# Optimization experiments

Hardware: AMD Instinct MI355X
Metric: run time of the kernel (lower is better)

The kernel has to match this reference:

```python
import jax, jax.numpy as jnp
import numpy as np

LOCAL_RADIUS = 127          # block_len = 128
TOKENS_PER_BLOCK = 16       # global_seq_len = L // 16
NEG = -1e9


def _concat_3_blocks(x):
    # x: [B, nb, bl, H, d] -> [B, nb, 3*bl, H, d] (prev, cur, next block; zero-padded ends)
    p = jnp.pad(x, [(0, 0), (1, 1), (0, 0), (0, 0), (0, 0)])
    return jnp.concatenate([p[:, :-2], p[:, 1:-1], p[:, 2:]], axis=2)


def _softmax_with_extra_logit(x, axis=-1):
    m = jnp.maximum(jax.lax.stop_gradient(x.max(axis, keepdims=True)), 0)
    unnorm = jnp.exp(x - m)
    denom = unnorm.sum(axis, keepdims=True) + jnp.exp(-m)
    return unnorm / denom


def setup_inputs() -> dict:
    key = jax.random.key(0)
    ks = jax.random.split(key, 5)
    B, L, D, H, dh = 2, 4096, 1024, 16, 64
    return {
        "x": jax.random.normal(ks[0], (B, L, D), jnp.float32),
        "Wq": jax.random.normal(ks[1], (D, H, dh), jnp.float32) * 0.02,
        "Wk": jax.random.normal(ks[2], (D, H, dh), jnp.float32) * 0.02,
        "Wv": jax.random.normal(ks[3], (D, H, dh), jnp.float32) * 0.02,
        "Wo": jax.random.normal(ks[4], (H, dh, D), jnp.float32) * 0.02,
    }


def reference(x, Wq, Wk, Wv, Wo):
    B, L, D = x.shape
    H, dh = Wq.shape[1], Wq.shape[2]
    bl = LOCAL_RADIUS + 1                      # block_len = 128
    nb = L // bl                               # num_blocks
    G = L // TOKENS_PER_BLOCK                  # global (side) seq len

    q = jnp.einsum("bld,dhk->blhk", x, Wq) / jnp.sqrt(jnp.asarray(dh, x.dtype))
    k = jnp.einsum("bld,dhk->blhk", x, Wk)
    v = jnp.einsum("bld,dhk->blhk", x, Wv)

    # transient-global aggregates: sum token embeddings within each block of TOKENS_PER_BLOCK
    block_ids = jnp.arange(L) // TOKENS_PER_BLOCK          # [L]
    one_hot = jax.nn.one_hot(block_ids, G, dtype=x.dtype)  # [L, G]
    g = jnp.einsum("bld,lg->bgd", x, one_hot)              # [B, G, D]
    side_k = jnp.einsum("bgd,dhk->bghk", g, Wk)
    side_v = jnp.einsum("bgd,dhk->bghk", g, Wv)

    # split into blocks and build 3-block sliding window keys/values
    qb = q.reshape(B, nb, bl, H, dh)
    kb = _concat_3_blocks(k.reshape(B, nb, bl, H, dh))     # [B, nb, 3bl, H, dh]
    vb = _concat_3_blocks(v.reshape(B, nb, bl, H, dh))

    k_cat = jnp.concatenate(
        [kb, jnp.broadcast_to(side_k[:, None], (B, nb, G, H, dh))], axis=2)
    v_cat = jnp.concatenate(
        [vb, jnp.broadcast_to(side_v[:, None], (B, nb, G, H, dh))], axis=2)

    # logits: [B, nb, H, bl, 3bl+G]
    logits = jnp.einsum("bnqhd,bnkhd->bnhqk", qb, k_cat)

    # local mask: enforce |rel| <= local_radius and in-bounds key positions
    q_idx = jnp.arange(bl)[:, None]                        # [bl, 1]
    k_idx = jnp.arange(3 * bl)[None, :]                    # [1, 3bl]
    rel = k_idx - bl - q_idx                               # relative position
    b_idx = jnp.arange(nb)[:, None, None]                  # [nb, 1, 1]
    k_pos = (b_idx - 1) * bl + k_idx                       # absolute key position
    valid = (jnp.abs(rel) <= LOCAL_RADIUS) & (k_pos >= 0) & (k_pos < L)
    local_bias = jnp.where(valid, 0.0, NEG).astype(logits.dtype)  # [nb, bl, 3bl]
    side_bias = jnp.zeros((nb, bl, G), logits.dtype)
    bias = jnp.concatenate([local_bias, side_bias], axis=-1)      # [nb, bl, 3bl+G]
    logits = logits + bias[None, :, None]

    probs = _softmax_with_extra_logit(logits, axis=-1)
    y = jnp.einsum("bnhqk,bnkhd->bnqhd", probs, v_cat)
    y = y.reshape(B, L, H, dh)
    return jnp.einsum("blhk,hkd->bld", y, Wo)
```

## Files before the change

kernel.cpp:

```cpp
#include <hip/hip_runtime.h>
#include <stdint.h>

#define SC_LOG2E 0.18033688011112042f

typedef __attribute__((ext_vector_type(8))) short short8;
typedef __attribute__((ext_vector_type(4))) short short4v;
typedef __attribute__((ext_vector_type(4))) float f32x4;

__device__ __forceinline__ unsigned short f2bf(float f) {
  unsigned int u = __float_as_uint(f);
  u += 0x7fffu + ((u >> 16) & 1u);
  return (unsigned short)(u >> 16);
}

__device__ __forceinline__ float bf2f(unsigned short u) {
  return __uint_as_float(((unsigned int)u) << 16);
}

__device__ __forceinline__ void gload_lds16(const void* g, void* l) {
  __builtin_amdgcn_global_load_lds((const __attribute__((address_space(1))) void*)g,
                                   (__attribute__((address_space(3))) void*)l,
                                   16, 0, 0);
}

__device__ __forceinline__ f32x4 mfma16(short8 a, short8 b, f32x4 c) {
  return __builtin_amdgcn_mfma_f32_16x16x32_bf16(a, b, c, 0, 0, 0);
}

__device__ __forceinline__ short4v tr_read(const unsigned short* p) {
  short4v r;
  asm volatile("ds_read_b64_tr_b16 %0, %1"
               : "=v"(r)
               : "v"((const __attribute__((address_space(3))) unsigned short*)p));
  return r;
}

__device__ __forceinline__ short8 cat44(short4v lo, short4v hi) {
  return __builtin_shufflevector(lo, hi, 0, 1, 2, 3, 4, 5, 6, 7);
}

__global__ __launch_bounds__(256) void prep_k(
    const float* __restrict__ x, unsigned short* __restrict__ xb,
    const float* __restrict__ wq, const float* __restrict__ wk,
    const float* __restrict__ wv, const float* __restrict__ wo,
    unsigned short* __restrict__ wqkv_t, unsigned short* __restrict__ wo_t) {
  __shared__ float tile[64 * 65];
  int bid = blockIdx.x;
  if (bid < 512) {
    int gr = bid;
    int c4 = threadIdx.x;
    const float4* p = (const float4*)(x + (size_t)gr * 16384) + c4;
#pragma unroll
    for (int t = 0; t < 16; ++t) {
      float4 v = p[(size_t)t * 256];
      ushort4 o;
      o.x = f2bf(v.x); o.y = f2bf(v.y); o.z = f2bf(v.z); o.w = f2bf(v.w);
      ((ushort4*)xb)[(size_t)(gr * 16 + t) * 256 + c4] = o;
    }
  } else {
    int idx = bid - 512;
    int z = idx >> 8, rem = idx & 255;
    const float* src = (z == 0) ? wq : (z == 1) ? wk : (z == 2) ? wv : wo;
    unsigned short* dst = (z == 3) ? wo_t : (wqkv_t + (size_t)z * 1048576);
    float scale = (z == 0) ? SC_LOG2E : 1.0f;
    int tc = (rem & 15) * 64, tr = (rem >> 4) * 64;
    int cx = threadIdx.x & 63, ry = threadIdx.x >> 6;
#pragma unroll
    for (int i = 0; i < 16; ++i) {
      int r = ry + i * 4;
      tile[r * 65 + cx] = src[(size_t)(tr + r) * 1024 + tc + cx];
    }
    __syncthreads();
#pragma unroll
    for (int i = 0; i < 16; ++i) {
      int r = ry + i * 4;
      dst[(size_t)(tc + r) * 1024 + tr + cx] = f2bf(tile[cx * 65 + r] * scale);
    }
  }
}

__global__ __launch_bounds__(256) void side_sum_k(
    const unsigned short* __restrict__ qkvb, unsigned short* __restrict__ sidekv) {
  int gr = blockIdx.x;
  int c8 = threadIdx.x;
  const unsigned short* src = qkvb + (size_t)(gr * 16) * 3072 + 1024 + c8 * 8;
  float s[8];
#pragma unroll
  for (int j = 0; j < 8; ++j) s[j] = 0.f;
#pragma unroll
  for (int t = 0; t < 16; ++t) {
    short8 v = *(const short8*)(src + (size_t)t * 3072);
#pragma unroll
    for (int j = 0; j < 8; ++j) s[j] += bf2f((unsigned short)v[j]);
  }
  short8 o;
#pragma unroll
  for (int j = 0; j < 8; ++j) o[j] = (short)f2bf(s[j]);
  *(short8*)(sidekv + (size_t)gr * 2048 + c8 * 8) = o;
}

template <bool F32OUT>
__global__ __launch_bounds__(256) void gemm_bt_k(
    const unsigned short* __restrict__ A, const unsigned short* __restrict__ Bt,
    void* __restrict__ Cv, int M, int N, int K, int nbn) {
  __shared__ unsigned short Alds[128 * 64];
  __shared__ unsigned short Blds[128 * 64];
  int bid = blockIdx.x;
  int bm = bid / nbn, bn = bid % nbn;
  int lane = threadIdx.x & 63, wid = threadIdx.x >> 6;
  int wr = wid >> 1, wc = wid & 1;
  int l15 = lane & 15, lg = lane >> 4;

  f32x4 zero4 = {0.f, 0.f, 0.f, 0.f};
  f32x4 acc[4][4];
#pragma unroll
  for (int i = 0; i < 4; ++i)
#pragma unroll
    for (int j = 0; j < 4; ++j) acc[i][j] = zero4;

  int srow[4], scol[4];
#pragma unroll
  for (int i = 0; i < 4; ++i) {
    int seg = wid * 4 + i;
    int r = seg * 8 + (lane >> 3);
    srow[i] = r;
    scol[i] = ((lane & 7) ^ (r & 7)) * 8;
  }
  size_t arow0 = (size_t)bm * 128, brow0 = (size_t)bn * 128;

  int ksteps = K >> 6;
  for (int ks = 0; ks < ksteps; ++ks) {
    int k0 = ks << 6;
#pragma unroll
    for (int i = 0; i < 4; ++i) {
      gload_lds16(A + (arow0 + srow[i]) * K + k0 + scol[i],
                  (char*)Alds + (wid * 4 + i) * 1024);
      gload_lds16(Bt + (brow0 + srow[i]) * K + k0 + scol[i],
                  (char*)Blds + (wid * 4 + i) * 1024);
    }
    __syncthreads();
#pragma unroll
    for (int kk = 0; kk < 2; ++kk) {
      short8 af[4], bfr[4];
#pragma unroll
      for (int mi = 0; mi < 4; ++mi) {
        int r = wr * 64 + mi * 16 + l15;
        af[mi] = *(const short8*)((const char*)Alds + r * 128 +
                                  ((kk * 64 + lg * 16) ^ ((r & 7) << 4)));
      }
#pragma unroll
      for (int ni = 0; ni < 4; ++ni) {
        int r = wc * 64 + ni * 16 + l15;
        bfr[ni] = *(const short8*)((const char*)Blds + r * 128 +
                                   ((kk * 64 + lg * 16) ^ ((r & 7) << 4)));
      }
#pragma unroll
      for (int mi = 0; mi < 4; ++mi)
#pragma unroll
        for (int ni = 0; ni < 4; ++ni)
          acc[mi][ni] = mfma16(af[mi], bfr[ni], acc[mi][ni]);
    }
    __syncthreads();
  }
  int rq = lg << 2;
#pragma unroll
  for (int mi = 0; mi < 4; ++mi) {
    size_t row = arow0 + wr * 64 + mi * 16 + rq;
#pragma unroll
    for (int ni = 0; ni < 4; ++ni) {
      size_t col = brow0 + wc * 64 + ni * 16 + l15;
#pragma unroll
      for (int r = 0; r < 4; ++r) {
        if (F32OUT)
          ((float*)Cv)[(row + r) * N + col] = acc[mi][ni][r];
        else
          ((unsigned short*)Cv)[(row + r) * N + col] = f2bf(acc[mi][ni][r]);
      }
    }
  }
}

__global__ __launch_bounds__(256) void attn_k(
    const unsigned short* __restrict__ qkv,
    const unsigned short* __restrict__ side,
    unsigned short* __restrict__ y) {
  const int L = 4096, G = 256;
  __shared__ unsigned short K0[4096], V0[4096];
  __shared__ unsigned short K1[4096], V1[4096];
  __shared__ unsigned short Pt[4][1024];

  int bid = blockIdx.x;
  int n = bid & 31, h = (bid >> 5) & 15, b = bid >> 9;
  int lane = threadIdx.x & 63, wid = threadIdx.x >> 6;
  int l15 = lane & 15, lg = lane >> 4, rq = lg << 2;

  short8 qf[2][2];
  {
    size_t rowb = (size_t)b * L + n * 128 + wid * 32;
#pragma unroll
    for (int qt = 0; qt < 2; ++qt)
#pragma unroll
      for (int kk = 0; kk < 2; ++kk)
        qf[qt][kk] = *(const short8*)(qkv + (rowb + qt * 16 + l15) * 3072 +
                                      h * 64 + kk * 32 + lg * 8);
  }

  f32x4 zero4 = {0.f, 0.f, 0.f, 0.f};
  f32x4 accO[2][4], accSum[2];
#pragma unroll
  for (int qt = 0; qt < 2; ++qt) {
    accSum[qt] = zero4;
#pragma unroll
    for (int dt = 0; dt < 4; ++dt) accO[qt][dt] = zero4;
  }

  short8 onesf;
  {
    short o = (l15 == 0) ? (short)0x3F80 : (short)0;
    onesf = (short8){o, o, o, o, o, o, o, o};
  }

  int clo = (n == 0) ? 2 : 0, chi = (n == 31) ? 4 : 6;
  int nloc = chi - clo, goff = 6 - nloc;
  int m = nloc + 4;
  unsigned short* pt = Pt[wid];

  auto stage = [&](int c, unsigned short* Kl, unsigned short* Vl) {
    bool isg = c >= 6;
#pragma unroll
    for (int i = 0; i < 2; ++i) {
      int seg = wid * 2 + i;
      int r = seg * 8 + (lane >> 3);
      int sl = ((lane & 7) ^ (r & 7)) * 8;
      int S = seg * 8 + (lane >> 3);
      int di = S >> 4, ks = (S >> 3) & 1, lgg = (S >> 1) & 3, half = S & 1;
      int k = ks * 32 + lgg * 8 + half * 4 + ((lane & 7) >> 1);
      int d = di * 16 + (lane & 1) * 8;
      const unsigned short *ksrc, *vsrc;
      if (!isg) {
        int rowbase = b * L + (n - 1) * 128 + c * 64;
        ksrc = qkv + (size_t)(rowbase + r) * 3072 + 1024 + h * 64 + sl;
        vsrc = qkv + (size_t)(rowbase + k) * 3072 + 2048 + h * 64 + d;
      } else {
        int rowbase = b * G + (c - 6) * 64;
        ksrc = side + (size_t)(rowbase + r) * 2048 + h * 64 + sl;
        vsrc = side + (size_t)(rowbase + k) * 2048 + 1024 + h * 64 + d;
      }
      gload_lds16(ksrc, (char*)Kl + seg * 1024);
      gload_lds16(vsrc, (char*)Vl + seg * 1024);
    }
  };

  auto compute = [&](int c, const unsigned short* Kl, const unsigned short* Vl) {
    bool isg = c >= 6;
    int d0 = c * 64 - 128 - wid * 32;
    if (!isg) {
      if (d0 >= 159 || d0 <= -191) return;
    }
    bool partial = !isg && !(d0 >= -96 && d0 <= 64);

    f32x4 sacc[2][4];
#pragma unroll
    for (int qt = 0; qt < 2; ++qt)
#pragma unroll
      for (int kt = 0; kt < 4; ++kt) sacc[qt][kt] = zero4;
    __builtin_amdgcn_s_setprio(1);
#pragma unroll
    for (int kk = 0; kk < 2; ++kk) {
      short8 kf[4];
#pragma unroll
      for (int kt = 0; kt < 4; ++kt) {
        int r = kt * 16 + l15;
        kf[kt] = *(const short8*)((const char*)Kl + r * 128 +
                                  ((kk * 64 + lg * 16) ^ ((r & 7) << 4)));
      }
#pragma unroll
      for (int qt = 0; qt < 2; ++qt)
#pragma unroll
        for (int kt = 0; kt < 4; ++kt)
          sacc[qt][kt] = mfma16(qf[qt][kk], kf[kt], sacc[qt][kt]);
    }
    __builtin_amdgcn_s_setprio(0);
    if (partial) {
      int relc = d0 + l15 - rq;
#pragma unroll
      for (int qt = 0; qt < 2; ++qt)
#pragma unroll
        for (int kt = 0; kt < 4; ++kt)
#pragma unroll
          for (int r = 0; r < 4; ++r) {
            int rel = relc + kt * 16 - qt * 16 - r;
            sacc[qt][kt][r] =
                ((unsigned)(rel + 127) <= 254u) ? sacc[qt][kt][r] : -1e30f;
          }
    }
#pragma unroll
    for (int ks = 0; ks < 2; ++ks) {
#pragma unroll
      for (int qt = 0; qt < 2; ++qt)
#pragma unroll
        for (int k2 = 0; k2 < 2; ++k2) {
          int kt = ks * 2 + k2;
          ushort4 pk;
          pk.x = f2bf(__builtin_amdgcn_exp2f(sacc[qt][kt][0]));
          pk.y = f2bf(__builtin_amdgcn_exp2f(sacc[qt][kt][1]));
          pk.z = f2bf(__builtin_amdgcn_exp2f(sacc[qt][kt][2]));
          pk.w = f2bf(__builtin_amdgcn_exp2f(sacc[qt][kt][3]));
          *(ushort4*)(pt + (k2 * 8 + ((l15 >> 2) << 1) + qt) * 64 +
                      (l15 & 3) * 16 + rq) = pk;
        }
      asm volatile("s_waitcnt lgkmcnt(0)" ::: "memory");
      short4v palo[2], pahi[2], vlo[4], vhi[4];
#pragma unroll
      for (int qt = 0; qt < 2; ++qt) {
        const unsigned short* pb = pt + (lg * 4 + qt) * 64 + l15 * 4;
        palo[qt] = tr_read(pb);
        pahi[qt] = tr_read(pb + 128);
      }
#pragma unroll
      for (int dt = 0; dt < 4; ++dt) {
        const unsigned short* base =
            Vl + (((dt * 2 + ks) * 4 + lg) * 2) * 64 + l15 * 4;
        vlo[dt] = tr_read(base);
        vhi[dt] = tr_read(base + 64);
      }
      asm volatile("s_waitcnt lgkmcnt(0)" ::: "memory");
      __builtin_amdgcn_sched_barrier(0);
      __builtin_amdgcn_s_setprio(1);
#pragma unroll
      for (int qt = 0; qt < 2; ++qt) {
        short8 pa = cat44(palo[qt], pahi[qt]);
#pragma unroll
        for (int dt = 0; dt < 4; ++dt)
          accO[qt][dt] = mfma16(pa, cat44(vlo[dt], vhi[dt]), accO[qt][dt]);
        accSum[qt] = mfma16(pa, onesf, accSum[qt]);
      }
      __builtin_amdgcn_s_setprio(0);
    }
  };

  auto chunk_of = [&](int i) { return i < nloc ? i + clo : i + goff; };

  stage(chunk_of(0), K0, V0);
  __syncthreads();
  for (int i = 0; i < m; i += 2) {
    if (i + 1 < m) stage(chunk_of(i + 1), K1, V1);
    compute(chunk_of(i), K0, V0);
    __syncthreads();
    if (i + 1 >= m) break;
    if (i + 2 < m) stage(chunk_of(i + 2), K0, V0);
    compute(chunk_of(i + 1), K1, V1);
    __syncthreads();
  }

  size_t rowb = (size_t)b * L + n * 128 + wid * 32;
#pragma unroll
  for (int qt = 0; qt < 2; ++qt) {
    float inv[4];
#pragma unroll
    for (int r = 0; r < 4; ++r) {
      float s = __shfl(accSum[qt][r], lane & 48);
      inv[r] = 1.f / (1.f + s);
    }
#pragma unroll
    for (int dt = 0; dt < 4; ++dt) {
      int col = h * 64 + dt * 16 + l15;
#pragma unroll
      for (int r = 0; r < 4; ++r)
        y[(rowb + qt * 16 + rq + r) * 1024 + col] =
            f2bf(accO[qt][dt][r] * inv[r]);
    }
  }
}

extern "C" void kernel_launch(void* const* d_in, const int* in_sizes, int n_in,
                              void* d_out, int out_size, void* d_ws, size_t ws_size,
                              hipStream_t stream) {
  const float* x  = (const float*)d_in[0];
  const float* wq = (const float*)d_in[1];
  const float* wk = (const float*)d_in[2];
  const float* wv = (const float*)d_in[3];
  const float* wo = (const float*)d_in[4];
  char* ws = (char*)d_ws;
  const size_t MB = 1 << 20;
  unsigned short* xb     = (unsigned short*)(ws);
  unsigned short* wqkv_t = (unsigned short*)(ws + 17 * MB);
  unsigned short* wo_t   = (unsigned short*)(ws + 23 * MB);
  unsigned short* qkvb   = (unsigned short*)(ws + 25 * MB);
  unsigned short* sidekv = (unsigned short*)(ws + 73 * MB);
  unsigned short* yb     = xb;

  prep_k<<<1536, 256, 0, stream>>>(x, xb, wq, wk, wv, wo, wqkv_t, wo_t);
  gemm_bt_k<false><<<64 * 24, 256, 0, stream>>>(xb, wqkv_t, qkvb, 8192, 3072, 1024, 24);
  side_sum_k<<<512, 256, 0, stream>>>(qkvb, sidekv);
  attn_k<<<1024, 256, 0, stream>>>(qkvb, sidekv, yb);
  gemm_bt_k<true><<<64 * 8, 256, 0, stream>>>(yb, wo_t, d_out, 8192, 1024, 1024, 8);
}
```

Measured before the change: 157.2 us.

## Fuse side K/V block sums into QKV GEMM epilogue and pack bf16 converts

Removes the separate side_sum kernel and computes the 16-token group sums of K and V inside the QKV GEMM epilogue, reducing fp32 accumulators across rows with cross-lane shuffles. This saves one launch and a re-read of the K/V activations. The sums are now taken from the fp32 accumulators rather than from bf16-rounded values, which changes rounding slightly. The attention softmax also switches to the packed float2-to-bf16 conversion intrinsic when writing probabilities.

```diff
diff --git a/kernel.cpp b/kernel.cpp
--- a/kernel.cpp
+++ b/kernel.cpp
@@ -1,4 +1,5 @@
 #include <hip/hip_runtime.h>
+#include <hip/hip_bf16.h>
 #include <stdint.h>
 
 #define SC_LOG2E 0.18033688011112042f
@@ -13,8 +14,10 @@
   return (unsigned short)(u >> 16);
 }
 
-__device__ __forceinline__ float bf2f(unsigned short u) {
-  return __uint_as_float(((unsigned int)u) << 16);
+__device__ __forceinline__ unsigned int pkbf(float a, float b) {
+  union { __hip_bfloat162 h; unsigned int u; } cv;
+  cv.h = __float22bfloat162_rn(float2{a, b});
+  return cv.u;
 }
 
 __device__ __forceinline__ void gload_lds16(const void* g, void* l) {
@@ -79,30 +82,11 @@
   }
 }
 
-__global__ __launch_bounds__(256) void side_sum_k(
-    const unsigned short* __restrict__ qkvb, unsigned short* __restrict__ sidekv) {
-  int gr = blockIdx.x;
-  int c8 = threadIdx.x;
-  const unsigned short* src = qkvb + (size_t)(gr * 16) * 3072 + 1024 + c8 * 8;
-  float s[8];
-#pragma unroll
-  for (int j = 0; j < 8; ++j) s[j] = 0.f;
-#pragma unroll
-  for (int t = 0; t < 16; ++t) {
-    short8 v = *(const short8*)(src + (size_t)t * 3072);
-#pragma unroll
-    for (int j = 0; j < 8; ++j) s[j] += bf2f((unsigned short)v[j]);
-  }
-  short8 o;
-#pragma unroll
-  for (int j = 0; j < 8; ++j) o[j] = (short)f2bf(s[j]);
-  *(short8*)(sidekv + (size_t)gr * 2048 + c8 * 8) = o;
-}
-
-template <bool F32OUT>
+template <bool F32OUT, bool SIDE>
 __global__ __launch_bounds__(256) void gemm_bt_k(
     const unsigned short* __restrict__ A, const unsigned short* __restrict__ Bt,
-    void* __restrict__ Cv, int M, int N, int K, int nbn) {
+    void* __restrict__ Cv, int M, int N, int K, int nbn,
+    unsigned short* __restrict__ sidekv) {
   __shared__ unsigned short Alds[128 * 64];
   __shared__ unsigned short Blds[128 * 64];
   int bid = blockIdx.x;
@@ -175,6 +159,22 @@
           ((float*)Cv)[(row + r) * N + col] = acc[mi][ni][r];
         else
           ((unsigned short*)Cv)[(row + r) * N + col] = f2bf(acc[mi][ni][r]);
+      }
+    }
+  }
+  if (SIDE && bn >= 8) {
+    int gg = bm * 8 + wr * 4;
+    int colb = bn * 128 - 1024 + wc * 64;
+#pragma unroll
+    for (int mi = 0; mi < 4; ++mi) {
+#pragma unroll
+      for (int ni = 0; ni < 4; ++ni) {
+        float s = (acc[mi][ni][0] + acc[mi][ni][1]) +
+                  (acc[mi][ni][2] + acc[mi][ni][3]);
+        s += __shfl_xor(s, 16);
+        s += __shfl_xor(s, 32);
+        if (lg == 0)
+          sidekv[(size_t)(gg + mi) * 2048 + colb + ni * 16 + l15] = f2bf(s);
       }
     }
   }
@@ -301,13 +301,13 @@
 #pragma unroll
         for (int k2 = 0; k2 < 2; ++k2) {
           int kt = ks * 2 + k2;
-          ushort4 pk;
-          pk.x = f2bf(__builtin_amdgcn_exp2f(sacc[qt][kt][0]));
-          pk.y = f2bf(__builtin_amdgcn_exp2f(sacc[qt][kt][1]));
-          pk.z = f2bf(__builtin_amdgcn_exp2f(sacc[qt][kt][2]));
-          pk.w = f2bf(__builtin_amdgcn_exp2f(sacc[qt][kt][3]));
-          *(ushort4*)(pt + (k2 * 8 + ((l15 >> 2) << 1) + qt) * 64 +
-                      (l15 & 3) * 16 + rq) = pk;
+          uint2 pk;
+          pk.x = pkbf(__builtin_amdgcn_exp2f(sacc[qt][kt][0]),
+                      __builtin_amdgcn_exp2f(sacc[qt][kt][1]));
+          pk.y = pkbf(__builtin_amdgcn_exp2f(sacc[qt][kt][2]),
+                      __builtin_amdgcn_exp2f(sacc[qt][kt][3]));
+          *(uint2*)(pt + (k2 * 8 + ((l15 >> 2) << 1) + qt) * 64 +
+                    (l15 & 3) * 16 + rq) = pk;
         }
       asm volatile("s_waitcnt lgkmcnt(0)" ::: "memory");
       short4v palo[2], pahi[2], vlo[4], vhi[4];
@@ -391,8 +391,9 @@
   unsigned short* yb     = xb;
 
   prep_k<<<1536, 256, 0, stream>>>(x, xb, wq, wk, wv, wo, wqkv_t, wo_t);
-  gemm_bt_k<false><<<64 * 24, 256, 0, stream>>>(xb, wqkv_t, qkvb, 8192, 3072, 1024, 24);
-  side_sum_k<<<512, 256, 0, stream>>>(qkvb, sidekv);
+  gemm_bt_k<false, true><<<64 * 24, 256, 0, stream>>>(
+      xb, wqkv_t, qkvb, 8192, 3072, 1024, 24, sidekv);
   attn_k<<<1024, 256, 0, stream>>>(qkvb, sidekv, yb);
-  gemm_bt_k<true><<<64 * 8, 256, 0, stream>>>(yb, wo_t, d_out, 8192, 1024, 1024, 8);
-}
+  gemm_bt_k<true, false><<<64 * 8, 256, 0, stream>>>(
+      yb, wo_t, d_out, 8192, 1024, 1024, 8, nullptr);
+}
```

After: 153.5 us. -2.3%, faster.
